# Kernel optimization log

Hardware: AMD Instinct MI355X
Metric: run time of the kernel (lower is better)

## Reference

```python
import jax, jax.numpy as jnp
import numpy as np

B, T, D, H = 2, 2048, 1024, 16
DK = D // H  # 64, head dim (even, required by RoPE pairing)


def setup_inputs() -> dict:
    key = jax.random.key(0)
    ks = jax.random.split(key, 9)
    sc = 1.0 / np.sqrt(D)
    x = jax.random.normal(ks[0], (B, T, D), jnp.float32)
    wq = jax.random.normal(ks[1], (D, D), jnp.float32) * sc
    bq = jax.random.normal(ks[2], (D,), jnp.float32) * 0.01
    wk = jax.random.normal(ks[3], (D, D), jnp.float32) * sc
    bk = jax.random.normal(ks[4], (D,), jnp.float32) * 0.01
    wv = jax.random.normal(ks[5], (D, D), jnp.float32) * sc
    bv = jax.random.normal(ks[6], (D,), jnp.float32) * 0.01
    wo = jax.random.normal(ks[7], (D, D), jnp.float32) * sc
    bo = jax.random.normal(ks[8], (D,), jnp.float32) * 0.01
    # causal mask, True = masked (matches masked_fill semantics); dim==3 -> broadcast over heads
    attn_mask = jnp.triu(jnp.ones((T, T), dtype=bool), 1)[None]  # [1,T,T]
    return dict(x=x, wq=wq, bq=bq, wk=wk, bk=bk, wv=wv, bv=bv, wo=wo, bo=bo,
                attn_mask=attn_mask)


def _rope(xh, sin, cos):
    # xh: [B,H,T,DK]; sin/cos: [T,DK/2]
    x1 = xh[..., 0::2]
    x2 = xh[..., 1::2]
    return jnp.stack([x1 * cos - x2 * sin, x1 * sin + x2 * cos], axis=-1).reshape(xh.shape)


def reference(x, wq, bq, wk, bk, wv, bv, wo, bo, attn_mask):
    q = (x @ wq.T + bq).reshape(B, T, H, DK).transpose(0, 2, 1, 3)  # [B,H,T,DK]
    k = (x @ wk.T + bk).reshape(B, T, H, DK).transpose(0, 2, 1, 3)
    v = (x @ wv.T + bv).reshape(B, T, H, DK).transpose(0, 2, 1, 3)
    # RoPE (seq_offset = 0)
    theta = 10000.0 ** (jnp.arange(0, DK, 2, dtype=jnp.float32) / DK)  # [DK/2]
    pos = jnp.arange(T, dtype=jnp.float32)[:, None]                    # [T,1]
    ang = pos / theta                                                  # [T,DK/2]
    sin, cos = jnp.sin(ang), jnp.cos(ang)
    q = _rope(q, sin, cos)
    k = _rope(k, sin, cos)
    # fp32 stable attention (inputs already fp32)
    scores = jnp.einsum('bhtd,bhsd->bhts', q, k) / np.sqrt(DK)
    scores = jnp.where(attn_mask[:, None], -1e9, scores)  # mask broadcast over heads
    attn = jax.nn.softmax(scores, axis=-1)
    ctx = jnp.einsum('bhts,bhsd->bhtd', attn, v)
    ctx = ctx.transpose(0, 2, 1, 3).reshape(B, T, D)
    return ctx @ wo.T + bo
```

## Files before the change

### kernel.cpp

```cpp
#include <hip/hip_runtime.h>
#include <stdint.h>
#include <stddef.h>

#define T_ 2048
#define D_ 1024
#define H_ 16

typedef __attribute__((ext_vector_type(8))) short short8;
typedef __attribute__((ext_vector_type(4))) float f32x4;
typedef __attribute__((ext_vector_type(4))) short s16x4;

__device__ __forceinline__ unsigned short f2bf(float f){
  union { float f; unsigned u; } c; c.f = f;
  unsigned u = c.u;
  return (unsigned short)((u + 0x7fffu + ((u >> 16) & 1u)) >> 16);
}

__device__ __forceinline__ unsigned pk_bf16(float lo, float hi){
  unsigned r;
  asm("v_cvt_pk_bf16_f32 %0, %1, %2" : "=v"(r) : "v"(lo), "v"(hi));
  return r;
}

__device__ __forceinline__ float fexp2(float x){
#if __has_builtin(__builtin_amdgcn_exp2f)
  return __builtin_amdgcn_exp2f(x);
#else
  return exp2f(x);
#endif
}

__device__ __forceinline__ f32x4 mfma16(short8 a, short8 b, f32x4 c){
  return __builtin_amdgcn_mfma_f32_16x16x32_bf16(a, b, c, 0, 0, 0);
}

__device__ __forceinline__ void gload16(const void* g, void* l){
  __builtin_amdgcn_global_load_lds(
      (const __attribute__((address_space(1))) unsigned*)g,
      (__attribute__((address_space(3))) unsigned*)l, 16, 0, 0);
}

__global__ __launch_bounds__(256) void k_prep(const float* __restrict__ x,
    const float* __restrict__ wq, const float* __restrict__ wk,
    const float* __restrict__ wv, const float* __restrict__ wo,
    unsigned short* __restrict__ xb, unsigned short* __restrict__ wqkv,
    unsigned short* __restrict__ wob, float* __restrict__ tab)
{
  if (blockIdx.x < 256){
    int i = blockIdx.x * 256 + threadIdx.x;
    int t = i >> 5, p = i & 31;
    float ang = (float)t * powf(10000.0f, -(float)p * (1.0f / 32.0f));
    tab[i] = sinf(ang);
    tab[T_ * 32 + i] = cosf(ang);
  }
  const long long NX = 4194304LL, NW = 1048576LL;
  long long base = ((long long)blockIdx.x * 256 + threadIdx.x) * 8;
  const float* s; unsigned short* d;
  if (base < NX){ s = x + base; d = xb + base; }
  else if (base < NX + 3*NW){
    long long j = base - NX;
    if (j < NW) s = wq + j;
    else if (j < 2*NW) s = wk + (j - NW);
    else s = wv + (j - 2*NW);
    d = wqkv + j;
  } else if (base < NX + 4*NW){
    long long j = base - NX - 3*NW;
    s = wo + j; d = wob + j;
  } else return;
  float4 a = *(const float4*)s;
  float4 b = *(const float4*)(s + 4);
  union { unsigned u[4]; short8 v; } o;
  o.u[0] = pk_bf16(a.x, a.y);
  o.u[1] = pk_bf16(a.z, a.w);
  o.u[2] = pk_bf16(b.x, b.y);
  o.u[3] = pk_bf16(b.z, b.w);
  *(short8*)d = o.v;
}

__device__ __forceinline__ void gemm_core(const unsigned short* __restrict__ A,
    const unsigned short* __restrict__ Bm, int m0, int n0,
    unsigned short* lA, unsigned short* lB, f32x4 (&acc)[4][4])
{
  const int tid = threadIdx.x, lane = tid & 63, wave = tid >> 6;
  const int wr = wave >> 1, wc = wave & 1;
  for (int mi = 0; mi < 4; ++mi)
    for (int ni = 0; ni < 4; ++ni)
      acc[mi][ni] = (f32x4){0.f, 0.f, 0.f, 0.f};
  for (int k0 = 0; k0 < 1024; k0 += 64){
    __syncthreads();
#pragma unroll
    for (int p = 0; p < 4; ++p){
      int c = p * 256 + tid, r = c >> 3, s = c & 7;
      int gs = (s ^ (r & 7)) << 3;
      gload16(A + (size_t)(m0 + r) * 1024 + k0 + gs, lA + c * 8);
      gload16(Bm + (size_t)(n0 + r) * 1024 + k0 + gs, lB + c * 8);
    }
    __syncthreads();
#pragma unroll
    for (int kk = 0; kk < 2; ++kk){
      int kslot = kk * 4 + (lane >> 4);
      short8 af[4], bf[4];
#pragma unroll
      for (int mi = 0; mi < 4; ++mi){
        int row = wr * 64 + mi * 16 + (lane & 15);
        af[mi] = *(const short8*)(lA + row * 64 + ((kslot ^ (row & 7)) << 3));
      }
#pragma unroll
      for (int ni = 0; ni < 4; ++ni){
        int row = wc * 64 + ni * 16 + (lane & 15);
        bf[ni] = *(const short8*)(lB + row * 64 + ((kslot ^ (row & 7)) << 3));
      }
#pragma unroll
      for (int mi = 0; mi < 4; ++mi)
#pragma unroll
        for (int ni = 0; ni < 4; ++ni)
          acc[mi][ni] = mfma16(af[mi], bf[ni], acc[mi][ni]);
    }
  }
}

__global__ __launch_bounds__(256) void k_qkv(const unsigned short* __restrict__ xb,
    const unsigned short* __restrict__ wqkv,
    const float* __restrict__ bq, const float* __restrict__ bk, const float* __restrict__ bv,
    const float* __restrict__ tab,
    unsigned short* __restrict__ Qw, unsigned short* __restrict__ Kw,
    unsigned short* __restrict__ Vw)
{
  __shared__ alignas(16) unsigned short lA[128 * 64];
  __shared__ alignas(16) unsigned short lB[128 * 64];
  int m0 = blockIdx.y * 128, n0 = blockIdx.x * 128;
  f32x4 acc[4][4];
  gemm_core(xb, wqkv, m0, n0, lA, lB, acc);
  int lane = threadIdx.x & 63, wave = threadIdx.x >> 6;
  int wr = wave >> 1, wc = wave & 1;
  int mat = n0 >> 10;
  const float* bias = (mat == 0) ? bq : (mat == 1 ? bk : bv);
  const float* st = tab; const float* ct = tab + T_ * 32;
  if (mat < 2){
    unsigned short* Out = (mat == 0) ? Qw : Kw;
    float qs = (mat == 0) ? 0.18033688011116f : 1.0f;
    for (int mi = 0; mi < 4; ++mi){
      for (int ni = 0; ni < 4; ++ni){
        int col = n0 + wc * 64 + ni * 16 + (lane & 15);
        int nn = col & 1023, h = nn >> 6, dd = nn & 63;
        float bsv = bias[nn];
        f32x4 v4 = acc[mi][ni];
#pragma unroll
        for (int r = 0; r < 4; ++r){
          int m = m0 + wr * 64 + mi * 16 + ((lane >> 4) << 2) + r;
          int bb = m >> 11, t = m & 2047;
          float v = v4[r] + bsv;
          float u = __shfl_xor(v, 1);
          int p = dd >> 1;
          float sv = st[t * 32 + p], cv = ct[t * 32 + p];
          float res = (dd & 1) ? (u * sv + v * cv) : (v * cv - u * sv);
          Out[((size_t)(bb * H_ + h) * T_ + t) * 64 + dd] = f2bf(res * qs);
        }
      }
    }
  } else {
    for (int mi = 0; mi < 4; ++mi){
      for (int ni = 0; ni < 4; ++ni){
        int col = n0 + wc * 64 + ni * 16 + (lane & 15);
        int nn = col & 1023, h = nn >> 6, dd = nn & 63;
        float bsv = bias[nn];
        int mb = m0 + wr * 64 + mi * 16 + ((lane >> 4) << 2);
        int bb = mb >> 11, t = mb & 2047;
        f32x4 v4 = acc[mi][ni];
        s16x4 o;
#pragma unroll
        for (int r = 0; r < 4; ++r) o[r] = (short)f2bf(v4[r] + bsv);
        *(s16x4*)(Vw + ((size_t)((bb * H_ + h) * 64 + dd)) * T_ + t) = o;
      }
    }
  }
}

__global__ __launch_bounds__(256) void k_attn(const unsigned short* __restrict__ Qw,
    const unsigned short* __restrict__ Kw, const unsigned short* __restrict__ Vt_g,
    unsigned short* __restrict__ ctxb)
{
  __shared__ alignas(16) unsigned short Kl[128 * 64];
  __shared__ alignas(16) unsigned short Vl[64 * 128];
  int qt = (int)gridDim.y - 1 - (int)blockIdx.y;
  int bh = blockIdx.x;
  int tid = threadIdx.x, lane = tid & 63, wave = tid >> 6;
  const unsigned short* Qb = Qw + (size_t)bh * T_ * 64;
  const unsigned short* Kb = Kw + (size_t)bh * T_ * 64;
  const unsigned short* Vb = Vt_g + (size_t)bh * 64 * T_;
  int q0 = qt * 128 + wave * 32;

  short8 qf[2][2];
#pragma unroll
  for (int mi = 0; mi < 2; ++mi){
    const unsigned short* qp = Qb + (size_t)(q0 + mi * 16 + (lane & 15)) * 64 + ((lane >> 4) << 3);
    qf[mi][0] = *(const short8*)qp;
    qf[mi][1] = *(const short8*)(qp + 32);
  }
  float mr[2] = {-1e30f, -1e30f}, lr[2] = {0.f, 0.f};
  f32x4 acc_o[2][4];
#pragma unroll
  for (int mi = 0; mi < 2; ++mi)
#pragma unroll
    for (int df = 0; df < 4; ++df) acc_o[mi][df] = (f32x4){0.f, 0.f, 0.f, 0.f};

  const int src0 = ((lane >> 4) & 1) * 32 + (lane & 15);
  const int src1 = src0 + 16;
  const bool hiHalf = lane >= 32;

  int ntiles = qt + 1;
  for (int jt = 0; jt < ntiles; ++jt){
    int j0 = jt * 128;
    __syncthreads();
#pragma unroll
    for (int p = 0; p < 4; ++p){
      int c = p * 256 + tid, r = c >> 3, s = c & 7;
      gload16(Kb + (size_t)(j0 + r) * 64 + ((s ^ (r & 7)) << 3), Kl + c * 8);
    }
#pragma unroll
    for (int p = 0; p < 4; ++p){
      int c = p * 256 + tid, r = c >> 4, s = c & 15;
      gload16(Vb + (size_t)r * T_ + j0 + ((s ^ (r & 7)) << 3), Vl + c * 8);
    }
    __syncthreads();
    if (j0 > q0 + 31) continue;
    bool need_mask = (j0 + 127 > q0);

    f32x4 accs[2][8];
#pragma unroll
    for (int mi = 0; mi < 2; ++mi)
#pragma unroll
      for (int jf = 0; jf < 8; ++jf) accs[mi][jf] = (f32x4){0.f, 0.f, 0.f, 0.f};
#pragma unroll
    for (int kk = 0; kk < 2; ++kk){
      int kslot = kk * 4 + (lane >> 4);
      short8 kf[8];
#pragma unroll
      for (int jf = 0; jf < 8; ++jf){
        int row = jf * 16 + (lane & 15);
        kf[jf] = *(const short8*)(Kl + row * 64 + ((kslot ^ (row & 7)) << 3));
      }
#pragma unroll
      for (int mi = 0; mi < 2; ++mi)
#pragma unroll
        for (int jf = 0; jf < 8; ++jf)
          accs[mi][jf] = mfma16(kf[jf], qf[mi][kk], accs[mi][jf]);
    }

    unsigned w0[2][8], w1[2][8];
#pragma unroll
    for (int mi = 0; mi < 2; ++mi){
      int qa = q0 + mi * 16 + (lane & 15);
      float mx = -1e30f;
#pragma unroll
      for (int jf = 0; jf < 8; ++jf)
#pragma unroll
        for (int r = 0; r < 4; ++r){
          float sv = accs[mi][jf][r];
          if (need_mask){
            int ja = j0 + jf * 16 + ((lane >> 4) << 2) + r;
            if (ja > qa) sv = -1e30f;
          }
          accs[mi][jf][r] = sv;
          mx = fmaxf(mx, sv);
        }
      mx = fmaxf(mx, __shfl_xor(mx, 16));
      mx = fmaxf(mx, __shfl_xor(mx, 32));
      float mn = fmaxf(mr[mi], mx);
      float sc = fexp2(mr[mi] - mn);
      mr[mi] = mn;
      float rs = 0.f;
#pragma unroll
      for (int jf = 0; jf < 8; ++jf)
#pragma unroll
        for (int r = 0; r < 4; ++r){
          float pe = fexp2(accs[mi][jf][r] - mn);
          accs[mi][jf][r] = pe;
          rs += pe;
        }
      rs += __shfl_xor(rs, 16);
      rs += __shfl_xor(rs, 32);
      lr[mi] = lr[mi] * sc + rs;
#pragma unroll
      for (int df = 0; df < 4; ++df){
        f32x4 a = acc_o[mi][df];
        a[0] *= sc; a[1] *= sc; a[2] *= sc; a[3] *= sc;
        acc_o[mi][df] = a;
      }
#pragma unroll
      for (int jf = 0; jf < 8; ++jf){
        w0[mi][jf] = pk_bf16(accs[mi][jf][0], accs[mi][jf][1]);
        w1[mi][jf] = pk_bf16(accs[mi][jf][2], accs[mi][jf][3]);
      }
    }

#pragma unroll
    for (int kk = 0; kk < 4; ++kk){
      int jslot = kk * 4 + (lane >> 4);
      short8 vf[4];
#pragma unroll
      for (int df = 0; df < 4; ++df){
        int row = df * 16 + (lane & 15);
        vf[df] = *(const short8*)(Vl + row * 128 + ((jslot ^ (row & 7)) << 3));
      }
#pragma unroll
      for (int mi = 0; mi < 2; ++mi){
        unsigned lo0 = (unsigned)__shfl((int)w0[mi][2*kk],   src0);
        unsigned hi0 = (unsigned)__shfl((int)w0[mi][2*kk+1], src0);
        unsigned lo1 = (unsigned)__shfl((int)w1[mi][2*kk],   src0);
        unsigned hi1 = (unsigned)__shfl((int)w1[mi][2*kk+1], src0);
        unsigned lo2 = (unsigned)__shfl((int)w0[mi][2*kk],   src1);
        unsigned hi2 = (unsigned)__shfl((int)w0[mi][2*kk+1], src1);
        unsigned lo3 = (unsigned)__shfl((int)w1[mi][2*kk],   src1);
        unsigned hi3 = (unsigned)__shfl((int)w1[mi][2*kk+1], src1);
        union { unsigned u[4]; short8 v; } pb;
        pb.u[0] = hiHalf ? hi0 : lo0;
        pb.u[1] = hiHalf ? hi1 : lo1;
        pb.u[2] = hiHalf ? hi2 : lo2;
        pb.u[3] = hiHalf ? hi3 : lo3;
#pragma unroll
        for (int df = 0; df < 4; ++df)
          acc_o[mi][df] = mfma16(vf[df], pb.v, acc_o[mi][df]);
      }
    }
  }

  int bb = bh >> 4, h = bh & 15;
#pragma unroll
  for (int mi = 0; mi < 2; ++mi){
    float inv = 1.0f / lr[mi];
    int t = q0 + mi * 16 + (lane & 15);
#pragma unroll
    for (int df = 0; df < 4; ++df){
      int d0 = df * 16 + ((lane >> 4) << 2);
      f32x4 a = acc_o[mi][df];
      s16x4 o;
#pragma unroll
      for (int r = 0; r < 4; ++r) o[r] = (short)f2bf(a[r] * inv);
      *(s16x4*)(ctxb + ((size_t)(bb * T_ + t)) * 1024 + h * 64 + d0) = o;
    }
  }
}

__global__ __launch_bounds__(256) void k_oproj(const unsigned short* __restrict__ ctxb,
    const unsigned short* __restrict__ wob, const float* __restrict__ bo,
    float* __restrict__ out)
{
  __shared__ alignas(16) unsigned short lA[128 * 64];
  __shared__ alignas(16) unsigned short lB[128 * 64];
  int m0 = blockIdx.y * 128, n0 = blockIdx.x * 128;
  f32x4 acc[4][4];
  gemm_core(ctxb, wob, m0, n0, lA, lB, acc);
  int lane = threadIdx.x & 63, wave = threadIdx.x >> 6;
  int wr = wave >> 1, wc = wave & 1;
  for (int mi = 0; mi < 4; ++mi)
    for (int ni = 0; ni < 4; ++ni){
      int col = n0 + wc * 64 + ni * 16 + (lane & 15);
      float bsv = bo[col];
      f32x4 v4 = acc[mi][ni];
#pragma unroll
      for (int r = 0; r < 4; ++r){
        int m = m0 + wr * 64 + mi * 16 + ((lane >> 4) << 2) + r;
        out[(size_t)m * 1024 + col] = v4[r] + bsv;
      }
    }
}

extern "C" void kernel_launch(void* const* d_in, const int* in_sizes, int n_in,
                              void* d_out, int out_size, void* d_ws, size_t ws_size,
                              hipStream_t stream)
{
  const float* x  = (const float*)d_in[0];
  const float* wq = (const float*)d_in[1];
  const float* bq = (const float*)d_in[2];
  const float* wk = (const float*)d_in[3];
  const float* bk = (const float*)d_in[4];
  const float* wv = (const float*)d_in[5];
  const float* bv = (const float*)d_in[6];
  const float* wo = (const float*)d_in[7];
  const float* bo = (const float*)d_in[8];
  char* w = (char*)d_ws;
  unsigned short* xb   = (unsigned short*)(w);
  unsigned short* wqkv = (unsigned short*)(w + (8 << 20));
  unsigned short* wob  = (unsigned short*)(w + (14 << 20));
  unsigned short* Qw   = (unsigned short*)(w + (16 << 20));
  unsigned short* Kw   = (unsigned short*)(w + (24 << 20));
  unsigned short* Vw   = (unsigned short*)(w + (32 << 20));
  unsigned short* ctxb = (unsigned short*)(w + (40 << 20));
  float* tab           = (float*)(w + (48 << 20));

  k_prep<<<4096, 256, 0, stream>>>(x, wq, wk, wv, wo, xb, wqkv, wob, tab);
  k_qkv<<<dim3(24, 32), 256, 0, stream>>>(xb, wqkv, bq, bk, bv, tab, Qw, Kw, Vw);
  k_attn<<<dim3(32, 16), 256, 0, stream>>>(Qw, Kw, Vw, ctxb);
  k_oproj<<<dim3(8, 32), 256, 0, stream>>>(ctxb, wob, bo, (float*)d_out);
}
```

Measured before the change: 141.0 us.

## Double-buffer K/V tiles in attention kernel to overlap loads with compute

The attention kernel now keeps two LDS buffers for K and V. It issues the global-to-LDS loads for the next tile before computing the current one, with one waitcnt+barrier per iteration instead of two syncthreads. The aim is to hide global memory latency behind MFMA work. LDS use doubles to 64KB per block, which may reduce occupancy.

Result: faster. 136.4 us (-3.3%).

```diff
diff --git a/kernel.cpp b/kernel.cpp
--- a/kernel.cpp
+++ b/kernel.cpp
@@ -180,8 +180,10 @@
     const unsigned short* __restrict__ Kw, const unsigned short* __restrict__ Vt_g,
     unsigned short* __restrict__ ctxb)
 {
-  __shared__ alignas(16) unsigned short Kl[128 * 64];
-  __shared__ alignas(16) unsigned short Vl[64 * 128];
+  __shared__ alignas(16) unsigned short Kl0[128 * 64];
+  __shared__ alignas(16) unsigned short Vl0[64 * 128];
+  __shared__ alignas(16) unsigned short Kl1[128 * 64];
+  __shared__ alignas(16) unsigned short Vl1[64 * 128];
   int qt = (int)gridDim.y - 1 - (int)blockIdx.y;
   int bh = blockIdx.x;
   int tid = threadIdx.x, lane = tid & 63, wave = tid >> 6;
@@ -208,24 +210,21 @@
   const int src1 = src0 + 16;
   const bool hiHalf = lane >= 32;
 
-  int ntiles = qt + 1;
-  for (int jt = 0; jt < ntiles; ++jt){
-    int j0 = jt * 128;
-    __syncthreads();
+  auto STAGE = [&](int j0, unsigned short* Kd, unsigned short* Vd){
 #pragma unroll
     for (int p = 0; p < 4; ++p){
       int c = p * 256 + tid, r = c >> 3, s = c & 7;
-      gload16(Kb + (size_t)(j0 + r) * 64 + ((s ^ (r & 7)) << 3), Kl + c * 8);
+      gload16(Kb + (size_t)(j0 + r) * 64 + ((s ^ (r & 7)) << 3), Kd + c * 8);
     }
 #pragma unroll
     for (int p = 0; p < 4; ++p){
       int c = p * 256 + tid, r = c >> 4, s = c & 15;
-      gload16(Vb + (size_t)r * T_ + j0 + ((s ^ (r & 7)) << 3), Vl + c * 8);
-    }
-    __syncthreads();
-    if (j0 > q0 + 31) continue;
+      gload16(Vb + (size_t)r * T_ + j0 + ((s ^ (r & 7)) << 3), Vd + c * 8);
+    }
+  };
+
+  auto COMPUTE = [&](int j0, const unsigned short* Kc, const unsigned short* Vc){
     bool need_mask = (j0 + 127 > q0);
-
     f32x4 accs[2][8];
 #pragma unroll
     for (int mi = 0; mi < 2; ++mi)
@@ -238,7 +237,7 @@
 #pragma unroll
       for (int jf = 0; jf < 8; ++jf){
         int row = jf * 16 + (lane & 15);
-        kf[jf] = *(const short8*)(Kl + row * 64 + ((kslot ^ (row & 7)) << 3));
+        kf[jf] = *(const short8*)(Kc + row * 64 + ((kslot ^ (row & 7)) << 3));
       }
 #pragma unroll
       for (int mi = 0; mi < 2; ++mi)
@@ -301,7 +300,7 @@
 #pragma unroll
       for (int df = 0; df < 4; ++df){
         int row = df * 16 + (lane & 15);
-        vf[df] = *(const short8*)(Vl + row * 128 + ((jslot ^ (row & 7)) << 3));
+        vf[df] = *(const short8*)(Vc + row * 128 + ((jslot ^ (row & 7)) << 3));
       }
 #pragma unroll
       for (int mi = 0; mi < 2; ++mi){
@@ -323,6 +322,22 @@
           acc_o[mi][df] = mfma16(vf[df], pb.v, acc_o[mi][df]);
       }
     }
+  };
+
+  int ntiles = qt + 1;
+  STAGE(0, Kl0, Vl0);
+  asm volatile("s_waitcnt vmcnt(0)" ::: "memory");
+  __builtin_amdgcn_s_barrier();
+  for (int jt = 0; jt < ntiles; ++jt){
+    bool ev = !(jt & 1);
+    unsigned short* Kc = ev ? Kl0 : Kl1;
+    unsigned short* Vc = ev ? Vl0 : Vl1;
+    if (jt + 1 < ntiles)
+      STAGE((jt + 1) * 128, ev ? Kl1 : Kl0, ev ? Vl1 : Vl0);
+    if (jt * 128 <= q0 + 31)
+      COMPUTE(jt * 128, Kc, Vc);
+    asm volatile("s_waitcnt vmcnt(0)" ::: "memory");
+    __builtin_amdgcn_s_barrier();
   }
 
   int bb = bh >> 4, h = bh & 15;
```
